# Optimization experiments

Measured on AMD Instinct MI355X. Metric: run time of the kernel, lower is better.

## Reference

```python
import jax, jax.numpy as jnp
import numpy as np

N_DIRS = 4
MAX_ITER = 5
GAMMA_MNODE = 2.0  # min_sum gamma_mnode from Params


def setup_inputs() -> dict:
    key = jax.random.key(0)
    B, H, W, L = 4, 256, 512, 21
    phi_i = jax.random.uniform(key, (B, H, W, L), dtype=jnp.float32) * 10.0  # unary costs
    eye = jnp.eye(L, dtype=jnp.float32)
    label_context = jnp.tile((1.0 - eye)[None], (N_DIRS, 1, 1))  # Potts init per __init__
    return {"phi_i": phi_i, "label_context": label_context}


def _sweep(unary, ctx):
    # unary: [S, B, R, L]; min-sum scanline recurrence along S (forward).
    # m_s(l') = min_l( unary_{s-1}(l) + m_{s-1}(l) + ctx(l, l') ), m_0 = 0.
    def step(m, u):
        tot = u + m  # [B, R, L]
        m_new = jnp.min(tot[..., :, None] + ctx, axis=-2)  # min over source label l
        m_new = m_new - jnp.min(m_new, axis=-1, keepdims=True)  # message normalization
        return m_new, m_new

    B, R, L = unary.shape[1:]
    init = jnp.zeros((B, R, L), unary.dtype)
    _, msgs = jax.lax.scan(step, init, unary[:-1])
    return jnp.concatenate([init[None], msgs], axis=0)  # [S, B, R, L]


def _dir_message(unary, ctx, d):
    # unary: [B, H, W, L]; d in {0: L->R, 1: R->L, 2: T->B, 3: B->T} (dir 0-3 of get_mode_params)
    if d == 0:
        u = jnp.transpose(unary, (2, 0, 1, 3))  # [W, B, H, L]
        m = _sweep(u, ctx)
        return jnp.transpose(m, (1, 2, 0, 3))
    if d == 1:
        u = jnp.transpose(unary[:, :, ::-1], (2, 0, 1, 3))
        m = _sweep(u, ctx)
        return jnp.transpose(m, (1, 2, 0, 3))[:, :, ::-1]
    if d == 2:
        u = jnp.transpose(unary, (1, 0, 2, 3))  # [H, B, W, L]
        m = _sweep(u, ctx)
        return jnp.transpose(m, (1, 0, 2, 3))
    u = jnp.transpose(unary[:, ::-1], (1, 0, 2, 3))
    m = _sweep(u, ctx)
    return jnp.transpose(m, (1, 0, 2, 3))[:, ::-1]


def reference(phi_i, label_context):
    # ISGMR-parallel min-sum directional message passing over a 2D grid.
    B, H, W, L = phi_i.shape
    msgs = jnp.zeros((N_DIRS, B, H, W, L), phi_i.dtype)
    for _ in range(MAX_ITER):
        total = phi_i + msgs.sum(0)  # aggregated cost
        msgs = jnp.stack(
            [_dir_message(total - msgs[d], label_context[d], d) for d in range(N_DIRS)], 0
        )
    # update_unary_belief (min_sum branch): phi_i * gamma_mnode + sum of messages
    unary_belief = phi_i * GAMMA_MNODE + msgs.sum(0)
    return unary_belief
```

## Files before the change

### kernel.cpp

```cpp
#include <hip/hip_runtime.h>

#define BB 4
#define HH 256
#define WW 512
#define LL 21
#define PIX (BB*HH*WW)
#define MSL 24
#define TSL 24
#define MFLD ((size_t)PIX*MSL)

#define CH 128
#define HA 32
#define FDV 32
#define HB 16

typedef float    fvec4 __attribute__((ext_vector_type(4)));
typedef _Float16 hvec4 __attribute__((ext_vector_type(4)));
typedef _Float16 hvec8 __attribute__((ext_vector_type(8)));
typedef unsigned uvec4 __attribute__((ext_vector_type(4)));

__device__ __forceinline__ fvec4 load4u(const float* p) {
    fvec4 v; __builtin_memcpy(&v, p, 16); return v;
}
__device__ __forceinline__ void store4u(float* p, fvec4 v) {
    __builtin_memcpy(p, &v, 16);
}

__global__ __launch_bounds__(256) void pad_kernel(
    const float* __restrict__ phi, _Float16* __restrict__ tot)
{
    int p = blockIdx.x * 256 + threadIdx.x;
    const float* pp = phi + (size_t)p * LL;
    float r[24];
    fvec4 u0 = load4u(pp + 0), u1 = load4u(pp + 4), u2 = load4u(pp + 8);
    fvec4 u3 = load4u(pp + 12), u4 = load4u(pp + 16);
    #pragma unroll
    for (int e = 0; e < 4; ++e) {
        r[e] = u0[e]; r[4+e] = u1[e]; r[8+e] = u2[e];
        r[12+e] = u3[e]; r[16+e] = u4[e];
    }
    r[20] = pp[20];
    r[21] = r[22] = r[23] = 0.f;

    _Float16* op = tot + (size_t)p * TSL;
    #pragma unroll
    for (int c3 = 0; c3 < 3; ++c3) {
        hvec8 h;
        #pragma unroll
        for (int e = 0; e < 8; ++e) h[e] = (_Float16)r[8*c3 + e];
        *(hvec8*)(op + 8*c3) = h;
    }
}

__global__ __launch_bounds__(256) void ewise_kernel(
    const float* __restrict__ phi, const unsigned char* __restrict__ msgs,
    const float* __restrict__ scales,
    float* __restrict__ outf, _Float16* __restrict__ outh,
    float scale, int padded_out)
{
    int p = blockIdx.x * 256 + threadIdx.x;
    const float* pp = phi + (size_t)p * LL;

    float r[24];
    {
        fvec4 u0 = load4u(pp + 0), u1 = load4u(pp + 4), u2 = load4u(pp + 8);
        fvec4 u3 = load4u(pp + 12), u4 = load4u(pp + 16);
        #pragma unroll
        for (int e = 0; e < 4; ++e) {
            r[e]      = u0[e] * scale;
            r[4 + e]  = u1[e] * scale;
            r[8 + e]  = u2[e] * scale;
            r[12 + e] = u3[e] * scale;
            r[16 + e] = u4[e] * scale;
        }
        r[20] = pp[20] * scale;
        r[21] = r[22] = r[23] = 0.f;
    }

    fvec4 sc = load4u(scales);

    #pragma unroll
    for (int d = 0; d < 4; ++d) {
        const unsigned* mp =
            (const unsigned*)(msgs + (size_t)d * MFLD + (size_t)p * MSL);
        uint2 w0 = *(const uint2*)(mp + 0);
        uint2 w1 = *(const uint2*)(mp + 2);
        uint2 w2 = *(const uint2*)(mp + 4);
        unsigned w[6] = { w0.x, w0.y, w1.x, w1.y, w2.x, w2.y };
        float rs = sc[d] * (1.f / 255.f);
        #pragma unroll
        for (int j = 0; j < 21; ++j)
            r[j] += (float)((w[j >> 2] >> ((j & 3) * 8)) & 0xffu) * rs;
    }

    if (padded_out) {
        _Float16* op = outh + (size_t)p * TSL;
        r[21] = r[22] = r[23] = 0.f;
        #pragma unroll
        for (int c3 = 0; c3 < 3; ++c3) {
            hvec8 h;
            #pragma unroll
            for (int e = 0; e < 8; ++e) h[e] = (_Float16)r[8*c3 + e];
            *(hvec8*)(op + 8*c3) = h;
        }
    } else {
        float* op = outf + (size_t)p * LL;
        store4u(op + 0,  *(const fvec4*)(r + 0));
        store4u(op + 4,  *(const fvec4*)(r + 4));
        store4u(op + 8,  *(const fvec4*)(r + 8));
        store4u(op + 12, *(const fvec4*)(r + 12));
        store4u(op + 16, *(const fvec4*)(r + 16));
        op[20] = r[20];
    }
}

__device__ __forceinline__ float min8(float x)
{
    int xi = __float_as_int(x); int y;
    y = __builtin_amdgcn_update_dpp(xi, xi, 0xB1, 0xf, 0xf, false);
    x = fminf(x, __int_as_float(y)); xi = __float_as_int(x);
    y = __builtin_amdgcn_update_dpp(xi, xi, 0x4E, 0xf, 0xf, false);
    x = fminf(x, __int_as_float(y)); xi = __float_as_int(x);
    y = __builtin_amdgcn_update_dpp(xi, xi, 0x141, 0xf, 0xf, false);
    x = fminf(x, __int_as_float(y));
    return x;
}
__device__ __forceinline__ float max8(float x)
{
    int xi = __float_as_int(x); int y;
    y = __builtin_amdgcn_update_dpp(xi, xi, 0xB1, 0xf, 0xf, false);
    x = fmaxf(x, __int_as_float(y)); xi = __float_as_int(x);
    y = __builtin_amdgcn_update_dpp(xi, xi, 0x4E, 0xf, 0xf, false);
    x = fmaxf(x, __int_as_float(y)); xi = __float_as_int(x);
    y = __builtin_amdgcn_update_dpp(xi, xi, 0x141, 0xf, 0xf, false);
    x = fmaxf(x, __int_as_float(y));
    return x;
}

template<bool FIRST>
__global__ __launch_bounds__(64) void sweep_kernel(
    const _Float16* __restrict__ tot, const float* __restrict__ ctx,
    unsigned char* __restrict__ msgs, float* __restrict__ scales)
{
    __shared__ float shc[LL * LL];
    __shared__ float shrm[LL];
    __shared__ float sht[8][MSL];
    __shared__ __align__(16) unsigned char ltot[2][8][800];
    __shared__ __align__(16) unsigned char lmsg[2][8][416];
    __shared__ __align__(16) unsigned char lout[8][416];

    const int lane = threadIdx.x;
    const int g = lane >> 3, k = lane & 7;
    const bool hz = (blockIdx.x < 1024);

    int d, chunk, r;
    int tstr, mstr;
    size_t pbase;
    if (hz) {
        int cl = blockIdx.x * 8 + g;
        chunk = cl >> 11;
        int line = cl & 2047;
        d = line >> 10;
        r = line & 1023;
        pbase = (size_t)r * WW;
        tstr = TSL; mstr = MSL;
        if (d == 1) { pbase += WW - 1; tstr = -tstr; mstr = -mstr; }
    } else {
        int cl = (blockIdx.x - 1024) * 8 + g;
        chunk = cl >> 12;
        int line = cl & 4095;
        d = 2 + (line >> 11);
        r = line & 2047;
        int bb = r >> 9, w = r & 511;
        pbase = (size_t)bb * HH * WW + w;
        tstr = WW * TSL; mstr = WW * MSL;
        if (d == 3) { pbase += (size_t)(HH - 1) * WW; tstr = -tstr; mstr = -mstr; }
    }
    const int ss = (chunk == 0) ? 0 : HA;
    const int sw = (chunk == 0) ? 0 : chunk * CH - HA;

    const float* ctxd = ctx + d * (LL * LL);
    const float  c    = ctxd[1];

    bool bad = (c < 0.f);
    float cmx = -1e30f, cmn = 1e30f;
    #pragma unroll
    for (int e = 0; e < 4; ++e) {
        int j = 4 * k + e;
        if (j < LL) {
            for (int l = 0; l < LL; ++l) {
                float v = ctxd[l * LL + j];
                float want = (l == j) ? 0.f : c;
                if (v != want) bad = true;
                cmx = fmaxf(cmx, v); cmn = fminf(cmn, v);
            }
        }
    }
    const bool potts = (__ballot(bad) == 0ull);
    const float R    = fmaxf(max8(cmx) - min8(cmn), 0.f);
    const float s255 = (R > 0.f) ? 255.f / R : 0.f;
    const float rs   = R * (1.f / 255.f);

    if (FIRST && lane == 0) scales[d] = R;

    const bool act = (k < 6);
    const bool okA = (k < 6);
    const bool okB = (k < 5);
    const int  koff = act ? 4 * k : 0;
    const bool dpos = ((d & 1) == 0);

    if (potts && hz) {
        const int r0 = r - g;
        const int sl = lane & 7;
        const int lg = lane >> 3;
        const char* tlineb = (const char*)tot
                             + (size_t)(r0 + sl) * ((size_t)WW * TSL * 2);
        unsigned char* mlineb = msgs + (size_t)d * MFLD
                              + (size_t)(r0 + sl) * ((size_t)WW * MSL);

        const int NB  = (ss + CH) / HB;
        const int swb = ss / HB;

        uvec4 rt[6]; uvec4 rm[3];
        auto wpix = [&](int b) {
            return dpos ? (sw + HB * b) : (496 - sw - HB * b);
        };
        auto issue = [&](int b) {
            int wp = wpix(b);
            const char* tb = tlineb + (size_t)wp * 48 + lg * 16;
            #pragma unroll
            for (int t = 0; t < 6; ++t) rt[t] = *(const uvec4*)(tb + t * 128);
            if (!FIRST) {
                const unsigned char* mb2 = mlineb + (size_t)wp * 24 + lg * 16;
                #pragma unroll
                for (int t = 0; t < 3; ++t) rm[t] = *(const uvec4*)(mb2 + t * 128);
            }
        };
        auto commit = [&](int b) {
            unsigned char* Lt = &ltot[b & 1][sl][0] + lg * 16;
            #pragma unroll
            for (int t = 0; t < 6; ++t) *(uvec4*)(Lt + t * 128) = rt[t];
            if (!FIRST) {
                unsigned char* Lm = &lmsg[b & 1][sl][0] + lg * 16;
                #pragma unroll
                for (int t = 0; t < 3; ++t) *(uvec4*)(Lm + t * 128) = rm[t];
            }
        };
        auto flushb = [&](int b) {
            int wp = wpix(b);
            unsigned char* mb2 = mlineb + (size_t)wp * 24 + lg * 16;
            const unsigned char* Lo = &lout[sl][0] + lg * 16;
            #pragma unroll
            for (int t = 0; t < 3; ++t)
                *(uvec4*)(mb2 + t * 128) = *(const uvec4*)(Lo + t * 128);
        };

        float mn0 = 0.f, mn1 = 0.f, mn2 = 0.f, mn3 = 0.f, tminp = 0.f;

        auto hstep = [&](const unsigned char* Lt, const unsigned char* Lm,
                         int p, bool st) {
            if (st && act) {
                float off = fmaf(-tminp, s255, 0.5f);
                unsigned q0 = (unsigned)fmaf(mn0, s255, off);
                unsigned q1 = (unsigned)fmaf(mn1, s255, off);
                unsigned q2 = (unsigned)fmaf(mn2, s255, off);
                unsigned q3 = (unsigned)fmaf(mn3, s255, off);
                *(unsigned*)(&lout[g][0] + p * 24 + 4 * k) =
                    q0 | (q1 << 8) | (q2 << 16) | (q3 << 24);
            }
            hvec4 th = *(const hvec4*)(Lt + p * 48 + 2 * koff);
            float T0, T1, T2, T3;
            if (FIRST) {
                T0 = (float)th[0] + mn0; T1 = (float)th[1] + mn1;
                T2 = (float)th[2] + mn2; T3 = (float)th[3] + mn3;
            } else {
                unsigned wd = *(const unsigned*)(Lm + p * 24 + koff);
                T0 = fmaf(-rs, (float)( wd        & 0xffu), (float)th[0]) + mn0;
                T1 = fmaf(-rs, (float)((wd >>  8) & 0xffu), (float)th[1]) + mn1;
                T2 = fmaf(-rs, (float)((wd >> 16) & 0xffu), (float)th[2]) + mn2;
                T3 = fmaf(-rs, (float)( wd >> 24        ), (float)th[3]) + mn3;
            }
            T0 = okA ? T0 : 1e30f;
            T1 = okB ? T1 : 1e30f;
            T2 = okB ? T2 : 1e30f;
            T3 = okB ? T3 : 1e30f;
            float lm = fminf(fminf(T0, T1), fminf(T2, T3));
            lm = min8(lm);
            float Q = lm + c;
            mn0 = fminf(T0, Q); mn1 = fminf(T1, Q);
            mn2 = fminf(T2, Q); mn3 = fminf(T3, Q);
            tminp = lm;
        };

        issue(0); commit(0);
        if (NB > 1) issue(1);
        for (int b = 0; b < NB; ++b) {
            const bool st = (b >= swb);
            const unsigned char* Lt = &ltot[b & 1][g][0];
            const unsigned char* Lm = &lmsg[b & 1][g][0];
            if (dpos) {
                #pragma unroll
                for (int i = 0; i < HB; ++i) hstep(Lt, Lm, i, st);
            } else {
                #pragma unroll
                for (int i = 0; i < HB; ++i) hstep(Lt, Lm, HB - 1 - i, st);
            }
            if (st) flushb(b);
            if (b + 1 < NB) {
                commit(b + 1);
                if (b + 2 < NB) issue(b + 2);
            }
        }
    } else if (potts) {
        const _Float16* tp = tot + pbase * TSL + koff + (ptrdiff_t)sw * tstr;
        unsigned char*  mb = msgs + (size_t)d * MFLD + pbase * MSL + koff
                                  + (ptrdiff_t)sw * mstr;

        hvec4 tf[FDV]; unsigned mfq[FDV];
        #pragma unroll
        for (int i = 0; i < FDV; ++i) {
            tf[i] = *(const hvec4*)(tp + (ptrdiff_t)i * tstr);
            mfq[i] = FIRST ? 0u : *(const unsigned*)(mb + (ptrdiff_t)i * mstr);
        }
        const _Float16* tld = tp + (ptrdiff_t)FDV * tstr;
        const unsigned char* mld = mb + (ptrdiff_t)FDV * mstr;
        unsigned char* mst = mb;

        float mn0 = 0.f, mn1 = 0.f, mn2 = 0.f, mn3 = 0.f, tminp = 0.f;

        auto vstep = [&](hvec4 th, unsigned wd, bool st) {
            if (st && act) {
                float off = fmaf(-tminp, s255, 0.5f);
                unsigned q0 = (unsigned)fmaf(mn0, s255, off);
                unsigned q1 = (unsigned)fmaf(mn1, s255, off);
                unsigned q2 = (unsigned)fmaf(mn2, s255, off);
                unsigned q3 = (unsigned)fmaf(mn3, s255, off);
                *(unsigned*)mst = q0 | (q1 << 8) | (q2 << 16) | (q3 << 24);
            }
            mst += mstr;
            float T0, T1, T2, T3;
            if (FIRST) {
                T0 = (float)th[0] + mn0; T1 = (float)th[1] + mn1;
                T2 = (float)th[2] + mn2; T3 = (float)th[3] + mn3;
            } else {
                T0 = fmaf(-rs, (float)( wd        & 0xffu), (float)th[0]) + mn0;
                T1 = fmaf(-rs, (float)((wd >>  8) & 0xffu), (float)th[1]) + mn1;
                T2 = fmaf(-rs, (float)((wd >> 16) & 0xffu), (float)th[2]) + mn2;
                T3 = fmaf(-rs, (float)( wd >> 24        ), (float)th[3]) + mn3;
            }
            T0 = okA ? T0 : 1e30f;
            T1 = okB ? T1 : 1e30f;
            T2 = okB ? T2 : 1e30f;
            T3 = okB ? T3 : 1e30f;
            float lm = fminf(fminf(T0, T1), fminf(T2, T3));
            lm = min8(lm);
            float Q = lm + c;
            mn0 = fminf(T0, Q); mn1 = fminf(T1, Q);
            mn2 = fminf(T2, Q); mn3 = fminf(T3, Q);
            tminp = lm;
        };

        const int nout = (ss + CH - FDV) / FDV;
        for (int j = 0; j < nout; ++j) {
            const bool st = (FDV * j >= ss);
            #pragma unroll
            for (int i = 0; i < FDV; ++i) {
                hvec4 th = tf[i]; unsigned wd = mfq[i];
                tf[i] = *(const hvec4*)tld;
                if (!FIRST) mfq[i] = *(const unsigned*)mld;
                tld += tstr; mld += mstr;
                vstep(th, wd, st);
            }
        }
        #pragma unroll
        for (int i = 0; i < FDV; ++i) vstep(tf[i], mfq[i], true);
    } else {
        for (int i = lane; i < LL * LL; i += 64) shc[i] = ctxd[i];
        __syncthreads();
        if (lane < LL) {
            float mn = shc[lane * LL];
            for (int j = 1; j < LL; ++j) mn = fminf(mn, shc[lane * LL + j]);
            shrm[lane] = mn;
        }
        __syncthreads();

        const _Float16* tp = tot + pbase * TSL + koff + (ptrdiff_t)sw * tstr;
        const unsigned char* mld = msgs + (size_t)d * MFLD + pbase * MSL + koff
                                        + (ptrdiff_t)sw * mstr;
        unsigned char* mst = (unsigned char*)mld;

        float m0 = 0.f, m1 = 0.f, m2 = 0.f, m3 = 0.f;
        const int j0 = (4 * k     < LL) ? 4 * k     : LL - 1;
        const int j1 = (4 * k + 1 < LL) ? 4 * k + 1 : LL - 1;
        const int j2 = (4 * k + 2 < LL) ? 4 * k + 2 : LL - 1;
        const int j3 = (4 * k + 3 < LL) ? 4 * k + 3 : LL - 1;

        const int total = ss + CH;
        for (int t = 0; t < total; ++t) {
            const bool st = (t >= ss);
            if (st && act) {
                unsigned q0 = (unsigned)fminf(fmaf(m0, s255, 0.5f), 255.f);
                unsigned q1 = (unsigned)fminf(fmaf(m1, s255, 0.5f), 255.f);
                unsigned q2 = (unsigned)fminf(fmaf(m2, s255, 0.5f), 255.f);
                unsigned q3 = (unsigned)fminf(fmaf(m3, s255, 0.5f), 255.f);
                *(unsigned*)mst = q0 | (q1 << 8) | (q2 << 16) | (q3 << 24);
            }
            hvec4 th = *(const hvec4*)(tp + (ptrdiff_t)t * tstr);
            unsigned wd = FIRST ? 0u
                : *(const unsigned*)(mld + (ptrdiff_t)t * mstr);
            mst += mstr;
            float t0, t1, t2, t3;
            if (FIRST) {
                t0 = (float)th[0] + m0; t1 = (float)th[1] + m1;
                t2 = (float)th[2] + m2; t3 = (float)th[3] + m3;
            } else {
                t0 = fmaf(-rs, (float)( wd        & 0xffu), (float)th[0]) + m0;
                t1 = fmaf(-rs, (float)((wd >>  8) & 0xffu), (float)th[1]) + m1;
                t2 = fmaf(-rs, (float)((wd >> 16) & 0xffu), (float)th[2]) + m2;
                t3 = fmaf(-rs, (float)( wd >> 24        ), (float)th[3]) + m3;
            }
            __syncthreads();
            if (okA) sht[g][4 * k] = t0;
            if (okB) {
                sht[g][4 * k + 1] = t1;
                sht[g][4 * k + 2] = t2;
                sht[g][4 * k + 3] = t3;
            }
            __syncthreads();
            float mnA = 1e30f, mnB = 1e30f, mnC = 1e30f, mnD = 1e30f;
            float gm  = 1e30f;
            for (int l = 0; l < LL; ++l) {
                float tl = sht[g][l];
                mnA = fminf(mnA, tl + shc[l * LL + j0]);
                mnB = fminf(mnB, tl + shc[l * LL + j1]);
                mnC = fminf(mnC, tl + shc[l * LL + j2]);
                mnD = fminf(mnD, tl + shc[l * LL + j3]);
                gm  = fminf(gm,  tl + shrm[l]);
            }
            m0 = mnA - gm; m1 = mnB - gm; m2 = mnC - gm; m3 = mnD - gm;
        }
    }
}

extern "C" void kernel_launch(void* const* d_in, const int* in_sizes, int n_in,
                              void* d_out, int out_size, void* d_ws, size_t ws_size,
                              hipStream_t stream)
{
    (void)in_sizes; (void)n_in; (void)out_size; (void)ws_size;

    const float* phi = (const float*)d_in[0];
    const float* ctx = (const float*)d_in[1];
    float* out = (float*)d_out;

    unsigned char* msgs = (unsigned char*)d_ws;
    _Float16* totp = (_Float16*)((char*)d_ws + 4 * MFLD);
    float* scales  = (float*)((char*)totp + (size_t)PIX * TSL * sizeof(_Float16));

    const int EW_BLOCKS = PIX / 256;
    const int SW_BLOCKS = 2048;

    pad_kernel<<<EW_BLOCKS, 256, 0, stream>>>(phi, totp);

    sweep_kernel<true><<<SW_BLOCKS, 64, 0, stream>>>(totp, ctx, msgs, scales);

    for (int it = 1; it < 5; ++it) {
        ewise_kernel<<<EW_BLOCKS, 256, 0, stream>>>(phi, msgs, scales,
                                                    nullptr, totp, 1.0f, 1);
        sweep_kernel<false><<<SW_BLOCKS, 64, 0, stream>>>(totp, ctx, msgs, scales);
    }

    ewise_kernel<<<EW_BLOCKS, 256, 0, stream>>>(phi, msgs, scales,
                                                out, nullptr, 2.0f, 0);
}
```

Baseline: 468.3 us.

## Halve horizontal sweep block, aliase shared buffers, prefetch LDS before next commit

Reduces the horizontal sweep block from 16 to 8 pixels and packs all shared arrays into one aliased pool, so each block uses far less LDS and more blocks can be resident. The per-block loop now reads all LDS inputs into registers first, then commits the next buffer and issues the global loads for the block after that before doing the serial min-sum recurrence. This overlaps the staging traffic with compute. It also doubles the number of block iterations and flushes, and overlaps ctx scratch with the tot/msg staging buffers, which relies on correct ordering.

```diff
diff --git a/kernel.cpp b/kernel.cpp
--- a/kernel.cpp
+++ b/kernel.cpp
@@ -12,7 +12,7 @@
 #define CH 128
 #define HA 32
 #define FDV 32
-#define HB 16
+#define HB 8
 
 typedef float    fvec4 __attribute__((ext_vector_type(4)));
 typedef _Float16 hvec4 __attribute__((ext_vector_type(4)));
@@ -142,12 +142,13 @@
     const _Float16* __restrict__ tot, const float* __restrict__ ctx,
     unsigned char* __restrict__ msgs, float* __restrict__ scales)
 {
-    __shared__ float shc[LL * LL];
-    __shared__ float shrm[LL];
-    __shared__ float sht[8][MSL];
-    __shared__ __align__(16) unsigned char ltot[2][8][800];
-    __shared__ __align__(16) unsigned char lmsg[2][8][416];
-    __shared__ __align__(16) unsigned char lout[8][416];
+    __shared__ __align__(16) unsigned char pool[11648];
+    auto ltot = (unsigned char (*)[8][416])pool;
+    auto lmsg = (unsigned char (*)[8][208])(pool + 6656);
+    auto lout = (unsigned char (*)[208])(pool + 9984);
+    float* shc  = (float*)pool;
+    float* shrm = (float*)(pool + 1792);
+    auto   sht  = (float (*)[24])(pool + 1920);
 
     const int lane = threadIdx.x;
     const int g = lane >> 3, k = lane & 7;
@@ -214,102 +215,106 @@
         const int sl = lane & 7;
         const int lg = lane >> 3;
         const char* tlineb = (const char*)tot
-                             + (size_t)(r0 + sl) * ((size_t)WW * TSL * 2);
+                             + (size_t)(r0 + sl) * ((size_t)WW * 48);
         unsigned char* mlineb = msgs + (size_t)d * MFLD
-                              + (size_t)(r0 + sl) * ((size_t)WW * MSL);
+                              + (size_t)(r0 + sl) * ((size_t)WW * 24);
 
         const int NB  = (ss + CH) / HB;
         const int swb = ss / HB;
 
-        uvec4 rt[6]; uvec4 rm[3];
+        uvec4 rt0, rt1, rt2;
+        uvec4 rm0; uint2 rm1;
+
         auto wpix = [&](int b) {
-            return dpos ? (sw + HB * b) : (496 - sw - HB * b);
+            return dpos ? (sw + HB * b) : ((WW - HB) - sw - HB * b);
         };
         auto issue = [&](int b) {
             int wp = wpix(b);
-            const char* tb = tlineb + (size_t)wp * 48 + lg * 16;
-            #pragma unroll
-            for (int t = 0; t < 6; ++t) rt[t] = *(const uvec4*)(tb + t * 128);
+            const char* tb = tlineb + (size_t)wp * 48;
+            rt0 = *(const uvec4*)(tb + lg * 16);
+            rt1 = *(const uvec4*)(tb + 128 + lg * 16);
+            rt2 = *(const uvec4*)(tb + 256 + lg * 16);
             if (!FIRST) {
-                const unsigned char* mb2 = mlineb + (size_t)wp * 24 + lg * 16;
-                #pragma unroll
-                for (int t = 0; t < 3; ++t) rm[t] = *(const uvec4*)(mb2 + t * 128);
+                const unsigned char* mq = mlineb + (size_t)wp * 24;
+                rm0 = *(const uvec4*)(mq + lg * 16);
+                rm1 = *(const uint2*)(mq + 128 + lg * 8);
             }
         };
         auto commit = [&](int b) {
-            unsigned char* Lt = &ltot[b & 1][sl][0] + lg * 16;
-            #pragma unroll
-            for (int t = 0; t < 6; ++t) *(uvec4*)(Lt + t * 128) = rt[t];
+            unsigned char* Lt = &ltot[b & 1][sl][0];
+            *(uvec4*)(Lt + lg * 16)       = rt0;
+            *(uvec4*)(Lt + 128 + lg * 16) = rt1;
+            *(uvec4*)(Lt + 256 + lg * 16) = rt2;
             if (!FIRST) {
-                unsigned char* Lm = &lmsg[b & 1][sl][0] + lg * 16;
-                #pragma unroll
-                for (int t = 0; t < 3; ++t) *(uvec4*)(Lm + t * 128) = rm[t];
+                unsigned char* Lm = &lmsg[b & 1][sl][0];
+                *(uvec4*)(Lm + lg * 16)      = rm0;
+                *(uint2*)(Lm + 128 + lg * 8) = rm1;
             }
         };
         auto flushb = [&](int b) {
             int wp = wpix(b);
-            unsigned char* mb2 = mlineb + (size_t)wp * 24 + lg * 16;
-            const unsigned char* Lo = &lout[sl][0] + lg * 16;
-            #pragma unroll
-            for (int t = 0; t < 3; ++t)
-                *(uvec4*)(mb2 + t * 128) = *(const uvec4*)(Lo + t * 128);
+            unsigned char* mq = mlineb + (size_t)wp * 24;
+            const unsigned char* Lo = &lout[sl][0];
+            uvec4 a = *(const uvec4*)(Lo + lg * 16);
+            uint2 bq = *(const uint2*)(Lo + 128 + lg * 8);
+            *(uvec4*)(mq + lg * 16)      = a;
+            *(uint2*)(mq + 128 + lg * 8) = bq;
         };
 
         float mn0 = 0.f, mn1 = 0.f, mn2 = 0.f, mn3 = 0.f, tminp = 0.f;
 
-        auto hstep = [&](const unsigned char* Lt, const unsigned char* Lm,
-                         int p, bool st) {
-            if (st && act) {
-                float off = fmaf(-tminp, s255, 0.5f);
-                unsigned q0 = (unsigned)fmaf(mn0, s255, off);
-                unsigned q1 = (unsigned)fmaf(mn1, s255, off);
-                unsigned q2 = (unsigned)fmaf(mn2, s255, off);
-                unsigned q3 = (unsigned)fmaf(mn3, s255, off);
-                *(unsigned*)(&lout[g][0] + p * 24 + 4 * k) =
-                    q0 | (q1 << 8) | (q2 << 16) | (q3 << 24);
-            }
-            hvec4 th = *(const hvec4*)(Lt + p * 48 + 2 * koff);
-            float T0, T1, T2, T3;
-            if (FIRST) {
-                T0 = (float)th[0] + mn0; T1 = (float)th[1] + mn1;
-                T2 = (float)th[2] + mn2; T3 = (float)th[3] + mn3;
-            } else {
-                unsigned wd = *(const unsigned*)(Lm + p * 24 + koff);
-                T0 = fmaf(-rs, (float)( wd        & 0xffu), (float)th[0]) + mn0;
-                T1 = fmaf(-rs, (float)((wd >>  8) & 0xffu), (float)th[1]) + mn1;
-                T2 = fmaf(-rs, (float)((wd >> 16) & 0xffu), (float)th[2]) + mn2;
-                T3 = fmaf(-rs, (float)( wd >> 24        ), (float)th[3]) + mn3;
-            }
-            T0 = okA ? T0 : 1e30f;
-            T1 = okB ? T1 : 1e30f;
-            T2 = okB ? T2 : 1e30f;
-            T3 = okB ? T3 : 1e30f;
-            float lm = fminf(fminf(T0, T1), fminf(T2, T3));
-            lm = min8(lm);
-            float Q = lm + c;
-            mn0 = fminf(T0, Q); mn1 = fminf(T1, Q);
-            mn2 = fminf(T2, Q); mn3 = fminf(T3, Q);
-            tminp = lm;
-        };
-
         issue(0); commit(0);
-        if (NB > 1) issue(1);
+        issue(1);
         for (int b = 0; b < NB; ++b) {
             const bool st = (b >= swb);
             const unsigned char* Lt = &ltot[b & 1][g][0];
             const unsigned char* Lm = &lmsg[b & 1][g][0];
-            if (dpos) {
-                #pragma unroll
-                for (int i = 0; i < HB; ++i) hstep(Lt, Lm, i, st);
-            } else {
-                #pragma unroll
-                for (int i = 0; i < HB; ++i) hstep(Lt, Lm, HB - 1 - i, st);
+
+            hvec4 th8[HB]; unsigned wd8[HB];
+            #pragma unroll
+            for (int i = 0; i < HB; ++i) {
+                int p = dpos ? i : HB - 1 - i;
+                th8[i] = *(const hvec4*)(Lt + p * 48 + 2 * koff);
+                wd8[i] = FIRST ? 0u : *(const unsigned*)(Lm + p * 24 + koff);
+            }
+            if (b + 1 < NB) commit(b + 1);
+            if (b + 2 < NB) issue(b + 2);
+
+            #pragma unroll
+            for (int i = 0; i < HB; ++i) {
+                int p = dpos ? i : HB - 1 - i;
+                if (st && act) {
+                    float off = fmaf(-tminp, s255, 0.5f);
+                    unsigned q0 = (unsigned)fmaf(mn0, s255, off);
+                    unsigned q1 = (unsigned)fmaf(mn1, s255, off);
+                    unsigned q2 = (unsigned)fmaf(mn2, s255, off);
+                    unsigned q3 = (unsigned)fmaf(mn3, s255, off);
+                    *(unsigned*)(&lout[g][0] + p * 24 + 4 * k) =
+                        q0 | (q1 << 8) | (q2 << 16) | (q3 << 24);
+                }
+                hvec4 th = th8[i]; unsigned wd = wd8[i];
+                float T0, T1, T2, T3;
+                if (FIRST) {
+                    T0 = (float)th[0] + mn0; T1 = (float)th[1] + mn1;
+                    T2 = (float)th[2] + mn2; T3 = (float)th[3] + mn3;
+                } else {
+                    T0 = fmaf(-rs, (float)( wd        & 0xffu), (float)th[0]) + mn0;
+                    T1 = fmaf(-rs, (float)((wd >>  8) & 0xffu), (float)th[1]) + mn1;
+                    T2 = fmaf(-rs, (float)((wd >> 16) & 0xffu), (float)th[2]) + mn2;
+                    T3 = fmaf(-rs, (float)( wd >> 24        ), (float)th[3]) + mn3;
+                }
+                T0 = okA ? T0 : 1e30f;
+                T1 = okB ? T1 : 1e30f;
+                T2 = okB ? T2 : 1e30f;
+                T3 = okB ? T3 : 1e30f;
+                float lm = fminf(fminf(T0, T1), fminf(T2, T3));
+                lm = min8(lm);
+                float Q = lm + c;
+                mn0 = fminf(T0, Q); mn1 = fminf(T1, Q);
+                mn2 = fminf(T2, Q); mn3 = fminf(T3, Q);
+                tminp = lm;
             }
             if (st) flushb(b);
-            if (b + 1 < NB) {
-                commit(b + 1);
-                if (b + 2 < NB) issue(b + 2);
-            }
         }
     } else if (potts) {
         const _Float16* tp = tot + pbase * TSL + koff + (ptrdiff_t)sw * tstr;
```

New measurement: 457.2 us. 2.4% less time.
